# Optimization experiments

Hardware: AMD Instinct MI355X
Metric: run time of the kernel (lower is better)

## Reference

```python
import jax, jax.numpy as jnp
import numpy as np

DIM = 768
NUM_HEADS = 12
HEAD_DIM = DIM // NUM_HEADS
SCALE = HEAD_DIM ** -0.5


def setup_inputs() -> dict:
    key = jax.random.key(0)
    ks = jax.random.split(key, 12)
    B, N, C, H = 8, 1024, DIM, NUM_HEADS
    s = 0.02
    return {
        'q_in': jax.random.normal(ks[0], (B, N, C), jnp.float32),
        'kv_in': jax.random.normal(ks[1], (B, N, C), jnp.float32),
        'Wq': jax.random.normal(ks[2], (C, C), jnp.float32) * s,
        'Wk': jax.random.normal(ks[3], (C, C), jnp.float32) * s,
        'Wv': jax.random.normal(ks[4], (C, C), jnp.float32) * s,
        'Wp': jax.random.normal(ks[5], (C, C), jnp.float32) * s,
        'bp': jnp.zeros((C,), jnp.float32),
        'W_dy2': jax.random.normal(ks[6], (H, C), jnp.float32) * s,  # lf gate linear (out=H)
        'b_dy2': jnp.zeros((H,), jnp.float32),
        'W_dy': jax.random.normal(ks[7], (H, C), jnp.float32) * s,   # hf gate linear
        'b_dy': jnp.zeros((H,), jnp.float32),
        'lf_gamma': jnp.full((C,), 1e-5, jnp.float32),
        'hf_gamma': jnp.full((C,), 1e-5, jnp.float32),
        'star_scale': jnp.ones((1,), jnp.float32),
        'star_bias': jnp.zeros((1,), jnp.float32),
    }


def reference(q_in, kv_in, Wq, Wk, Wv, Wp, bp, W_dy2, b_dy2, W_dy, b_dy,
              lf_gamma, hf_gamma, star_scale, star_bias):
    B, Nq, C = q_in.shape
    Nk = kv_in.shape[1]
    H, D = NUM_HEADS, HEAD_DIM

    # StarReLU on query tokens (ignore_cls_token = 0)
    dy_feat = star_scale * jnp.square(jax.nn.relu(q_in)) + star_bias  # (B,Nq,C)

    # low-freq dynamic gate: tanh(linear) per head, repeated over head_dim
    dy_lf = jnp.tanh(jnp.einsum('bnc,hc->bnh', dy_feat, W_dy2) + b_dy2)  # (B,Nq,H)
    dy_lf = jnp.repeat(dy_lf, D, axis=-1)  # (B,Nq,C)

    # high-freq dynamic gate: rational-of-softplus^2
    dy = jax.nn.softplus(jnp.einsum('bnc,hc->bnh', dy_feat, W_dy) + b_dy)
    dy2 = jnp.square(dy)
    dy_hf = 2.0 * dy2 / (dy2 + 0.3678)
    dy_hf = jnp.repeat(dy_hf, D, axis=-1)  # (B,Nq,C)

    # projections (torch Linear: y = x @ W.T), split heads
    q = jnp.einsum('bnc,dc->bnd', q_in, Wq).reshape(B, Nq, H, D).transpose(0, 2, 1, 3)
    k = jnp.einsum('bnc,dc->bnd', kv_in, Wk).reshape(B, Nk, H, D).transpose(0, 2, 1, 3)
    v = jnp.einsum('bnc,dc->bnd', kv_in, Wv).reshape(B, Nk, H, D).transpose(0, 2, 1, 3)

    attn = jnp.einsum('bhqd,bhkd->bhqk', q * SCALE, k)
    attn = jax.nn.softmax(attn, axis=-1)
    x_attn = jnp.einsum('bhqk,bhkd->bhqd', attn, v)
    x_attn = x_attn.transpose(0, 2, 1, 3).reshape(B, Nq, C)

    # Nk == Nq branch: per-token residual high-frequency component
    v_reshape = v.transpose(0, 2, 1, 3).reshape(B, Nk, C)
    v_hf = v_reshape - x_attn

    x_attn = x_attn + x_attn * dy_lf * lf_gamma
    x_attn = x_attn + dy_hf * v_hf * hf_gamma

    out = jnp.einsum('bnc,dc->bnd', x_attn, Wp) + bp
    return out
```

## Files before the change

kernel.cpp:

```cpp
#include <hip/hip_runtime.h>
#include <hip/hip_bf16.h>
#include <stdint.h>

typedef unsigned short u16;
typedef unsigned int u32;
typedef unsigned long long u64;
typedef __attribute__((ext_vector_type(8))) short short8;
typedef __attribute__((ext_vector_type(4))) float f32x4;

#define LOG2E 1.44269504f

static __device__ __forceinline__ u16 f2bf(float f) {
    u32 x = __float_as_uint(f);
    u32 r = (x + 0x7FFFu + ((x >> 16) & 1u)) >> 16;
    return (u16)r;
}
static __device__ __forceinline__ float bf2f(u16 u) {
    return __uint_as_float(((u32)u) << 16);
}
static __device__ __forceinline__ u32 pk2(float lo, float hi) {
    __hip_bfloat162 t = __float22bfloat162_rn(float2{lo, hi});
    union { __hip_bfloat162 b; u32 u; } cv;
    cv.b = t;
    return cv.u;
}
static __device__ __forceinline__ float fexp2(float x) {
#if __has_builtin(__builtin_amdgcn_exp2f)
    return __builtin_amdgcn_exp2f(x);
#else
    return exp2f(x);
#endif
}

static __device__ __forceinline__ void g2l16(const void* g, void* l) {
    __builtin_amdgcn_global_load_lds((const __attribute__((address_space(1))) void*)g,
                                     (__attribute__((address_space(3))) void*)l, 16, 0, 0);
}

__global__ __launch_bounds__(256) void k_cvt_all(
    const float* __restrict__ q_in, const float* __restrict__ kv_in,
    const float* __restrict__ Wq, const float* __restrict__ Wk,
    const float* __restrict__ Wv, const float* __restrict__ Wp,
    const float* __restrict__ Wdy2, const float* __restrict__ Wdy,
    u16* __restrict__ qbf, u16* __restrict__ kvbf, u16* __restrict__ Wqb,
    u16* __restrict__ Wkb, u16* __restrict__ Wvb, u16* __restrict__ Wpb,
    u16* __restrict__ wgb) {
    int i = blockIdx.x * 256 + threadIdx.x;
    const float* src;
    u16* dst;
    int so, dofs;
    if (i < 786432) { src = q_in; dst = qbf; so = i; dofs = i; }
    else if (i < 1572864) { src = kv_in; dst = kvbf; so = i - 786432; dofs = so; }
    else if (i < 1646592) { src = Wq; dst = Wqb; so = i - 1572864; dofs = so; }
    else if (i < 1720320) { src = Wk; dst = Wkb; so = i - 1646592; dofs = so; }
    else if (i < 1794048) { src = Wv; dst = Wvb; so = i - 1720320; dofs = so; }
    else if (i < 1867776) { src = Wp; dst = Wpb; so = i - 1794048; dofs = so; }
    else if (i < 1870080) {
        int e = i - 1867776;
        dst = wgb; dofs = e;
        if (e < 1152) { src = Wdy2; so = e; }
        else { src = Wdy; so = e - 1152; }
    } else return;
    const float4* p = (const float4*)src + (size_t)so * 2;
    float4 a = p[0], b = p[1];
    short8 o;
    o[0] = f2bf(a.x); o[1] = f2bf(a.y); o[2] = f2bf(a.z); o[3] = f2bf(a.w);
    o[4] = f2bf(b.x); o[5] = f2bf(b.y); o[6] = f2bf(b.z); o[7] = f2bf(b.w);
    *((short8*)dst + dofs) = o;
}

__global__ __launch_bounds__(64) void k_gates(
    const u16* __restrict__ qbf, const u16* __restrict__ wgb,
    const float* __restrict__ bdy2, const float* __restrict__ bdy,
    const float* __restrict__ star_s, const float* __restrict__ star_b,
    float* __restrict__ glf, float* __restrict__ ghf) {
    int lane = threadIdx.x;
    int g = lane >> 4, c = lane & 15;
    int row0 = blockIdx.x * 16;
    float ss = star_s[0], sb = star_b[0];
    f32x4 acc[2];
    acc[0] = (f32x4){0.f, 0.f, 0.f, 0.f};
    acc[1] = (f32x4){0.f, 0.f, 0.f, 0.f};
    for (int t = 0; t < 24; ++t) {
        int k0 = t * 32;
        short8 x8 = *(const short8*)(qbf + (size_t)(row0 + c) * 768 + k0 + g * 8);
        float f[8];
#pragma unroll
        for (int j = 0; j < 8; ++j) {
            float x = fmaxf(bf2f((u16)x8[j]), 0.f);
            f[j] = ss * x * x + sb;
        }
        union { u32 u[4]; short8 s8; } au;
#pragma unroll
        for (int j = 0; j < 4; ++j) au.u[j] = pk2(f[2 * j], f[2 * j + 1]);
        short8 b0 = *(const short8*)(wgb + (size_t)c * 768 + k0 + g * 8);
        short8 b1 = (short8){0, 0, 0, 0, 0, 0, 0, 0};
        if (c < 8)
            b1 = *(const short8*)(wgb + (size_t)(16 + c) * 768 + k0 + g * 8);
        acc[0] = __builtin_amdgcn_mfma_f32_16x16x32_bf16(au.s8, b0, acc[0], 0, 0, 0);
        acc[1] = __builtin_amdgcn_mfma_f32_16x16x32_bf16(au.s8, b1, acc[1], 0, 0, 0);
    }
#pragma unroll
    for (int n = 0; n < 2; ++n)
#pragma unroll
        for (int r = 0; r < 4; ++r) {
            int token = row0 + g * 4 + r;
            int o = n * 16 + c;
            float v = acc[n][r];
            if (o < 12) {
                glf[(size_t)token * 12 + o] = tanhf(v + bdy2[o]);
            } else if (o < 24) {
                float x = v + bdy[o - 12];
                float sp = (x > 15.f) ? x : log1pf(expf(x));
                float d2 = sp * sp;
                ghf[(size_t)token * 12 + (o - 12)] = 2.f * d2 / (d2 + 0.3678f);
            }
        }
}

__device__ __forceinline__ void gemm_core(const u16* __restrict__ A,
                                          const u16* __restrict__ W, u16* As,
                                          u16* Bs, int rowA0, int rowB0,
                                          int lane, int w, int wm, int wn,
                                          f32x4 acc[4][4]) {
    int g = lane >> 4, c = lane & 15;
#pragma unroll
    for (int m = 0; m < 4; ++m)
#pragma unroll
        for (int n = 0; n < 4; ++n) acc[m][n] = (f32x4){0.f, 0.f, 0.f, 0.f};

    auto stage = [&](int buf, int k0) {
#pragma unroll
        for (int j = 0; j < 2; ++j) {
            int L = w * 128 + j * 64 + lane;
            int p = L >> 3, s8 = L & 7;
            int t2 = s8 ^ (p & 7);
            int row = 2 * p + (t2 >> 2);
            int chunk = t2 & 3;
            size_t go = (size_t)row * 768 + k0 + chunk * 8;
            g2l16(A + (size_t)rowA0 * 768 + go, As + buf * 4096 + L * 8);
            g2l16(W + (size_t)rowB0 * 768 + go, Bs + buf * 4096 + L * 8);
        }
    };

    stage(0, 0);
    stage(1, 32);
    int cur = 0, nxt = 2;
    for (int t = 0; t < 24; ++t) {
        if (t < 23) asm volatile("s_waitcnt vmcnt(4)" ::: "memory");
        else        asm volatile("s_waitcnt vmcnt(0)" ::: "memory");
        __builtin_amdgcn_s_barrier();
        if (t < 22) stage(nxt, (t + 2) * 32);
        short8 a[4], b[4];
#pragma unroll
        for (int m = 0; m < 4; ++m) {
            int row = wm * 64 + m * 16 + c;
            int off = (row >> 1) * 64 +
                      ((((row & 1) << 2) | g) ^ ((row >> 1) & 7)) * 8;
            a[m] = *(const short8*)(As + cur * 4096 + off);
        }
#pragma unroll
        for (int n = 0; n < 4; ++n) {
            int row = wn * 64 + n * 16 + c;
            int off = (row >> 1) * 64 +
                      ((((row & 1) << 2) | g) ^ ((row >> 1) & 7)) * 8;
            b[n] = *(const short8*)(Bs + cur * 4096 + off);
        }
        __builtin_amdgcn_s_setprio(1);
#pragma unroll
        for (int m = 0; m < 4; ++m)
#pragma unroll
            for (int n = 0; n < 4; ++n)
                acc[m][n] = __builtin_amdgcn_mfma_f32_16x16x32_bf16(
                    a[m], b[n], acc[m][n], 0, 0, 0);
        __builtin_amdgcn_s_setprio(0);
        cur = (cur == 2) ? 0 : cur + 1;
        nxt = (nxt == 2) ? 0 : nxt + 1;
    }
}

__global__ __launch_bounds__(256, 3) void k_gemm_qkv(
    const u16* __restrict__ qbf, const u16* __restrict__ kvbf,
    const u16* __restrict__ Wqb, const u16* __restrict__ Wkb,
    const u16* __restrict__ Wvb, u16* __restrict__ Qb, u16* __restrict__ Kb,
    u16* __restrict__ VTg, u16* __restrict__ vlin) {
    __shared__ __align__(16) u16 smem[24576];
    u16* As = smem;
    u16* Bs = smem + 12288;
    int bid = blockIdx.x;
    int logical = (bid & 7) * 144 + (bid >> 3);
    int panel = logical / 18, sub = logical % 18;
    int type = sub / 6, tn = sub % 6;
    int tid = threadIdx.x, lane = tid & 63, w = tid >> 6;
    int g = lane >> 4, c = lane & 15;
    int wm = w >> 1, wn = w & 1;
    int rowA0 = panel * 128, rowB0 = tn * 128;
    const u16* A = (type == 0) ? qbf : kvbf;
    const u16* W = (type == 0) ? Wqb : (type == 1) ? Wkb : Wvb;

    f32x4 acc[4][4];
    gemm_core(A, W, As, Bs, rowA0, rowB0, lane, w, wm, wn, acc);

    if (type == 0) {
        const float scl = 0.125f * LOG2E;
#pragma unroll
        for (int m = 0; m < 4; ++m)
#pragma unroll
            for (int n = 0; n < 4; ++n)
#pragma unroll
                for (int r = 0; r < 4; ++r) {
                    int row = rowA0 + wm * 64 + m * 16 + g * 4 + r;
                    int col = rowB0 + wn * 64 + n * 16 + c;
                    int bb = row >> 10, nn = row & 1023, hh = col >> 6,
                        dd = col & 63;
                    Qb[((size_t)(bb * 12 + hh) << 16) + (nn << 6) + dd] =
                        f2bf(acc[m][n][r] * scl);
                }
    } else if (type == 1) {
#pragma unroll
        for (int m = 0; m < 4; ++m)
#pragma unroll
            for (int n = 0; n < 4; ++n)
#pragma unroll
                for (int r = 0; r < 4; ++r) {
                    int row = rowA0 + wm * 64 + m * 16 + g * 4 + r;
                    int col = rowB0 + wn * 64 + n * 16 + c;
                    int bb = row >> 10, nn = row & 1023, hh = col >> 6,
                        dd = col & 63;
                    Kb[((size_t)(bb * 12 + hh) << 16) + (nn << 6) + dd] =
                        f2bf(acc[m][n][r]);
                }
    } else {
#pragma unroll
        for (int m = 0; m < 4; ++m)
#pragma unroll
            for (int n = 0; n < 4; ++n)
#pragma unroll
                for (int r = 0; r < 4; ++r) {
                    int row = rowA0 + wm * 64 + m * 16 + g * 4 + r;
                    int col = rowB0 + wn * 64 + n * 16 + c;
                    vlin[(size_t)row * 768 + col] = f2bf(acc[m][n][r]);
                }
        __syncthreads();
#pragma unroll
        for (int m = 0; m < 4; ++m)
#pragma unroll
            for (int n = 0; n < 4; ++n)
#pragma unroll
                for (int r = 0; r < 4; ++r) {
                    int rl = wm * 64 + m * 16 + g * 4 + r;
                    int cl = wn * 64 + n * 16 + c;
                    smem[cl * 128 + rl] = f2bf(acc[m][n][r]);
                }
        __syncthreads();
        int bb = rowA0 >> 10, nn0 = rowA0 & 1023;
#pragma unroll
        for (int j = 0; j < 8; ++j) {
            int idx = j * 256 + tid;
            int rT = idx >> 4, cc = idx & 15;
            int dout = rowB0 + rT, hh = dout >> 6, dd = dout & 63;
            const u16* srow = smem + rT * 128 + cc * 8;
            size_t robase = ((size_t)(bb * 12 + hh) * 64 + dd) * 1024;
#pragma unroll
            for (int e2 = 0; e2 < 4; ++e2) {
                int n0 = nn0 + cc * 8 + 2 * e2;
                int t6 = n0 & 63;
                int pos = (((t6 >> 1) & 1) << 5) | (((t6 >> 2) & 3) << 3) |
                          (((t6 >> 4) & 3) << 1) | (t6 & 1);
                u32 val = (u32)srow[2 * e2] | ((u32)srow[2 * e2 + 1] << 16);
                *(u32*)(VTg + robase + (n0 & ~63) + pos) = val;
            }
        }
    }
}

__global__ __launch_bounds__(256, 3) void k_gemm_out(
    const u16* __restrict__ xf, const u16* __restrict__ Wpb,
    const float* __restrict__ bp, float* __restrict__ out) {
    __shared__ __align__(16) u16 smem[24576];
    u16* As = smem;
    u16* Bs = smem + 12288;
    int bid = blockIdx.x;
    int logical = (bid & 7) * 48 + (bid >> 3);
    int c48 = logical % 48;
    int tm = (logical / 48) * 8 + c48 / 6, tn = c48 % 6;
    int tid = threadIdx.x, lane = tid & 63, w = tid >> 6;
    int wm = w >> 1, wn = w & 1;
    int rowA0 = tm * 128, rowB0 = tn * 128;

    f32x4 acc[4][4];
    gemm_core(xf, Wpb, As, Bs, rowA0, rowB0, lane, w, wm, wn, acc);

#pragma unroll
    for (int m = 0; m < 4; ++m)
#pragma unroll
        for (int n = 0; n < 4; ++n)
#pragma unroll
            for (int r = 0; r < 4; ++r) {
                int row = rowA0 + wm * 64 + m * 16 + (lane >> 4) * 4 + r;
                int col = rowB0 + wn * 64 + n * 16 + (lane & 15);
                out[(size_t)row * 768 + col] = acc[m][n][r] + bp[col];
            }
}

__global__ __launch_bounds__(256, 3) void k_attn(
    const u16* __restrict__ Qb, const u16* __restrict__ Kb,
    const u16* __restrict__ VTg, const u16* __restrict__ vlin,
    const float* __restrict__ glf, const float* __restrict__ ghf,
    const float* __restrict__ lfg, const float* __restrict__ hfg,
    u16* __restrict__ xfinal) {
    __shared__ __align__(16) u16 Ks[12288];
    __shared__ __align__(16) u16 Vs[12288];
    int b8 = blockIdx.x;
    int sw = (b8 & 7) * 96 + (b8 >> 3);
    int bh = sw >> 3, qblk = sw & 7;
    int bb = bh / 12, hh = bh % 12;
    int tid = threadIdx.x, lane = tid & 63, w = tid >> 6;
    int g = lane >> 4, c = lane & 15;
    const char* Kp = (const char*)(Kb + ((size_t)bh << 16));
    const char* Vp = (const char*)(VTg + ((size_t)bh << 16));
    const u16* Qp = Qb + ((size_t)bh << 16);
    int q0 = qblk * 128 + w * 32;

    short8 qf[2][2];
#pragma unroll
    for (int qb = 0; qb < 2; ++qb)
#pragma unroll
        for (int ks = 0; ks < 2; ++ks)
            qf[qb][ks] = *(const short8*)(Qp + (size_t)(q0 + qb * 16 + c) * 64 +
                                          ks * 32 + g * 8);

    f32x4 o[2][4];
#pragma unroll
    for (int qb = 0; qb < 2; ++qb)
#pragma unroll
        for (int n = 0; n < 4; ++n) o[qb][n] = (f32x4){0.f, 0.f, 0.f, 0.f};
    f32x4 o5[2];
    o5[0] = (f32x4){0.f, 0.f, 0.f, 0.f};
    o5[1] = (f32x4){0.f, 0.f, 0.f, 0.f};
    const short8 vones = (short8){(short)0x3F80, (short)0x3F80, (short)0x3F80,
                                  (short)0x3F80, (short)0x3F80, (short)0x3F80,
                                  (short)0x3F80, (short)0x3F80};

    int kgo[2], vgo[2], ldo[2];
#pragma unroll
    for (int h = 0; h < 2; ++h) {
        int idx = w * 64 + lane + h * 256;
        int row = idx >> 3;
        int colb = ((idx & 7) * 16) ^ ((row & 7) << 4);
        kgo[h] = row * 128 + colb;
        vgo[h] = row * 2048 + colb;
        ldo[h] = (w * 64 + h * 256) * 16;
    }

    auto stage = [&](int bi, int t) {
#pragma unroll
        for (int h = 0; h < 2; ++h) {
            g2l16(Kp + (size_t)t * 8192 + kgo[h], (char*)Ks + bi * 8192 + ldo[h]);
            g2l16(Vp + (size_t)t * 128 + vgo[h], (char*)Vs + bi * 8192 + ldo[h]);
        }
    };

    stage(0, 0);
    stage(1, 1);
    int cur = 0, nxt = 2;
    int cs = (c & 7) << 4;
    for (int t = 0; t < 16; ++t) {
        if (t < 15) asm volatile("s_waitcnt vmcnt(4)" ::: "memory");
        else        asm volatile("s_waitcnt vmcnt(0)" ::: "memory");
        __builtin_amdgcn_s_barrier();
        if (t < 14) stage(nxt, t + 2);
        const char* Kbase = (const char*)Ks + cur * 8192;
        const char* Vbase = (const char*)Vs + cur * 8192;
        short8 kf[4][2], vf[4][2];
#pragma unroll
        for (int m = 0; m < 4; ++m) {
            int rowb = (m * 16 + c) * 128;
#pragma unroll
            for (int ks = 0; ks < 2; ++ks)
                kf[m][ks] = *(const short8*)(Kbase + rowb +
                                             ((g * 16 + ks * 64) ^ cs));
        }
#pragma unroll
        for (int n = 0; n < 4; ++n) {
            int rowb = (n * 16 + c) * 128;
#pragma unroll
            for (int a = 0; a < 2; ++a)
                vf[n][a] = *(const short8*)(Vbase + rowb +
                                            ((a * 64 + g * 16) ^ cs));
        }
#pragma unroll
        for (int qb = 0; qb < 2; ++qb) {
            f32x4 s[4];
            __builtin_amdgcn_s_setprio(1);
#pragma unroll
            for (int m = 0; m < 4; ++m) {
                s[m] = __builtin_amdgcn_mfma_f32_16x16x32_bf16(
                    kf[m][0], qf[qb][0], (f32x4){0.f, 0.f, 0.f, 0.f}, 0, 0, 0);
                s[m] = __builtin_amdgcn_mfma_f32_16x16x32_bf16(
                    kf[m][1], qf[qb][1], s[m], 0, 0, 0);
            }
            __builtin_amdgcn_s_setprio(0);
            u32 P2[4][2];
#pragma unroll
            for (int m = 0; m < 4; ++m) {
#pragma unroll
                for (int r = 0; r < 4; ++r) s[m][r] = fexp2(s[m][r]);
                P2[m][0] = pk2(s[m][0], s[m][1]);
                P2[m][1] = pk2(s[m][2], s[m][3]);
            }
#pragma unroll
            for (int a = 0; a < 2; ++a) {
                union { u32 u[4]; short8 s8; } pu;
                pu.u[0] = P2[0][a]; pu.u[1] = P2[1][a];
                pu.u[2] = P2[2][a]; pu.u[3] = P2[3][a];
                __builtin_amdgcn_s_setprio(1);
#pragma unroll
                for (int n = 0; n < 4; ++n)
                    o[qb][n] = __builtin_amdgcn_mfma_f32_16x16x32_bf16(
                        pu.s8, vf[n][a], o[qb][n], 0, 0, 0);
                o5[qb] = __builtin_amdgcn_mfma_f32_16x16x32_bf16(
                    pu.s8, vones, o5[qb], 0, 0, 0);
                __builtin_amdgcn_s_setprio(0);
            }
        }
        cur = (cur == 2) ? 0 : cur + 1;
        nxt = (nxt == 2) ? 0 : nxt + 1;
    }
    __syncthreads();

    u16* X = &Ks[0];
#pragma unroll
    for (int qb = 0; qb < 2; ++qb) {
        float rl[4];
#pragma unroll
        for (int r = 0; r < 4; ++r) rl[r] = 1.0f / o5[qb][r];
#pragma unroll
        for (int n = 0; n < 4; ++n)
#pragma unroll
            for (int r = 0; r < 4; ++r) {
                int row = w * 32 + qb * 16 + 4 * g + r;
                int col = n * 16 + c;
                int byte = row * 128 + ((col * 2) ^ ((row & 3) << 4));
                *(u16*)((char*)X + byte) = f2bf(o[qb][n][r] * rl[r]);
            }
    }
    __syncthreads();
    {
        int row = tid >> 1, half = tid & 1;
        size_t token = (size_t)bb * 1024 + qblk * 128 + row;
        float alf = glf[token * 12 + hh];
        float ahf = ghf[token * 12 + hh];
        int dbase = hh * 64 + half * 32;
        const u16* vbase = vlin + token * 768 + dbase;
        u16* obase = xfinal + token * 768 + dbase;
#pragma unroll
        for (int j = 0; j < 4; ++j) {
            int phys = ((half * 4 + j) ^ (row & 3)) * 16;
            short8 xa8 = *(const short8*)((char*)X + row * 128 + phys);
            short8 vl8 = *(const short8*)(vbase + j * 8);
            float4 lg0 = *(const float4*)(lfg + dbase + j * 8);
            float4 lg1 = *(const float4*)(lfg + dbase + j * 8 + 4);
            float4 hg0 = *(const float4*)(hfg + dbase + j * 8);
            float4 hg1 = *(const float4*)(hfg + dbase + j * 8 + 4);
            float lg[8] = {lg0.x, lg0.y, lg0.z, lg0.w, lg1.x, lg1.y, lg1.z, lg1.w};
            float hg[8] = {hg0.x, hg0.y, hg0.z, hg0.w, hg1.x, hg1.y, hg1.z, hg1.w};
            short8 oo;
#pragma unroll
            for (int e = 0; e < 8; ++e) {
                float xa = bf2f((u16)xa8[e]);
                float v = bf2f((u16)vl8[e]);
                float val = xa + xa * alf * lg[e] + ahf * (v - xa) * hg[e];
                oo[e] = f2bf(val);
            }
            *(short8*)(obase + j * 8) = oo;
        }
    }
}

extern "C" void kernel_launch(void* const* d_in, const int* in_sizes, int n_in,
                              void* d_out, int out_size, void* d_ws,
                              size_t ws_size, hipStream_t stream) {
    const float* q_in = (const float*)d_in[0];
    const float* kv_in = (const float*)d_in[1];
    const float* Wq = (const float*)d_in[2];
    const float* Wk = (const float*)d_in[3];
    const float* Wv = (const float*)d_in[4];
    const float* Wp = (const float*)d_in[5];
    const float* bp = (const float*)d_in[6];
    const float* Wdy2 = (const float*)d_in[7];
    const float* bdy2 = (const float*)d_in[8];
    const float* Wdy = (const float*)d_in[9];
    const float* bdy = (const float*)d_in[10];
    const float* lfg = (const float*)d_in[11];
    const float* hfg = (const float*)d_in[12];
    const float* st_s = (const float*)d_in[13];
    const float* st_b = (const float*)d_in[14];
    float* out = (float*)d_out;

    char* ws = (char*)d_ws;
    const size_t MC2 = (size_t)8192 * 768 * 2;
    const size_t WB = (size_t)768 * 768 * 2;
    u16* qbf = (u16*)(ws);
    u16* kvbf = (u16*)(ws + MC2);
    u16* Wqb = (u16*)(ws + 2 * MC2);
    u16* Wkb = (u16*)(ws + 2 * MC2 + WB);
    u16* Wvb = (u16*)(ws + 2 * MC2 + 2 * WB);
    u16* Wpb = (u16*)(ws + 2 * MC2 + 3 * WB);
    u16* Qb = (u16*)(ws + 2 * MC2 + 4 * WB);
    u16* Kb = (u16*)(ws + 3 * MC2 + 4 * WB);
    u16* VTg = (u16*)(ws + 4 * MC2 + 4 * WB);
    u16* vlin = (u16*)(ws + 5 * MC2 + 4 * WB);
    float* glf = (float*)(ws + 6 * MC2 + 4 * WB);
    float* ghf = (float*)(ws + 6 * MC2 + 4 * WB + (size_t)8192 * 12 * 4);
    u16* wgb = (u16*)(ws + 6 * MC2 + 4 * WB + (size_t)8192 * 12 * 8);
    u16* xfinal = qbf;

    k_cvt_all<<<7305, 256, 0, stream>>>(q_in, kv_in, Wq, Wk, Wv, Wp, Wdy2,
                                        Wdy, qbf, kvbf, Wqb, Wkb, Wvb, Wpb,
                                        wgb);
    k_gates<<<512, 64, 0, stream>>>(qbf, wgb, bdy2, bdy, st_s, st_b, glf, ghf);
    k_gemm_qkv<<<1152, 256, 0, stream>>>(qbf, kvbf, Wqb, Wkb, Wvb, Qb, Kb,
                                         VTg, vlin);
    k_attn<<<768, 256, 0, stream>>>(Qb, Kb, VTg, vlin, glf, ghf, lfg, hfg,
                                    xfinal);
    k_gemm_out<<<384, 256, 0, stream>>>(xfinal, Wpb, bp, out);
}
```

Before: 134.2 us.

## Fuse K and V projections to share kv_in tile loads in QKV GEMM

The K and V projection blocks now run together: each block loads one kv_in A tile and multiplies it against both Wk and Wv tiles, keeping two accumulator sets, so the kv_in activations are read once instead of twice. The grid shrinks from 1152 to 768 blocks. The GEMM pipeline also changes from triple-buffered prefetch with one barrier to double buffering with two barriers per k-step, and launch bounds drop from 3 to 2 blocks per SM. The doubled accumulators raise register pressure and lower occupancy, and the extra barrier may cost latency hiding in both the QKV and output GEMMs.

```diff
diff --git a/kernel.cpp b/kernel.cpp
--- a/kernel.cpp
+++ b/kernel.cpp
@@ -118,16 +118,17 @@
         }
 }
 
-__device__ __forceinline__ void gemm_core(const u16* __restrict__ A,
-                                          const u16* __restrict__ W, u16* As,
-                                          u16* Bs, int rowA0, int rowB0,
-                                          int lane, int w, int wm, int wn,
-                                          f32x4 acc[4][4]) {
+template <int NB>
+__device__ __forceinline__ void gemm_nb(const u16* __restrict__ A,
+                                        const u16* __restrict__ W0,
+                                        const u16* __restrict__ W1, u16* smem,
+                                        int rowA0, int rowB0, int lane, int w,
+                                        int wm, int wn, f32x4 acc0[4][4],
+                                        f32x4 acc1[4][4]) {
     int g = lane >> 4, c = lane & 15;
-#pragma unroll
-    for (int m = 0; m < 4; ++m)
-#pragma unroll
-        for (int n = 0; n < 4; ++n) acc[m][n] = (f32x4){0.f, 0.f, 0.f, 0.f};
+    u16* As = smem;
+    u16* B0 = smem + 8192;
+    u16* B1 = smem + 16384;
 
     auto stage = [&](int buf, int k0) {
 #pragma unroll
@@ -139,69 +140,88 @@
             int chunk = t2 & 3;
             size_t go = (size_t)row * 768 + k0 + chunk * 8;
             g2l16(A + (size_t)rowA0 * 768 + go, As + buf * 4096 + L * 8);
-            g2l16(W + (size_t)rowB0 * 768 + go, Bs + buf * 4096 + L * 8);
+            g2l16(W0 + (size_t)rowB0 * 768 + go, B0 + buf * 4096 + L * 8);
+            if (NB == 2)
+                g2l16(W1 + (size_t)rowB0 * 768 + go, B1 + buf * 4096 + L * 8);
         }
     };
 
     stage(0, 0);
-    stage(1, 32);
-    int cur = 0, nxt = 2;
+    int buf = 0;
     for (int t = 0; t < 24; ++t) {
-        if (t < 23) asm volatile("s_waitcnt vmcnt(4)" ::: "memory");
-        else        asm volatile("s_waitcnt vmcnt(0)" ::: "memory");
+        if (t < 23) stage(buf ^ 1, (t + 1) * 32);
+        if (t < 23) {
+            if (NB == 2) asm volatile("s_waitcnt vmcnt(6)" ::: "memory");
+            else         asm volatile("s_waitcnt vmcnt(4)" ::: "memory");
+        } else {
+            asm volatile("s_waitcnt vmcnt(0)" ::: "memory");
+        }
         __builtin_amdgcn_s_barrier();
-        if (t < 22) stage(nxt, (t + 2) * 32);
-        short8 a[4], b[4];
+        short8 a[4], b0[4], b1[4];
 #pragma unroll
         for (int m = 0; m < 4; ++m) {
             int row = wm * 64 + m * 16 + c;
             int off = (row >> 1) * 64 +
                       ((((row & 1) << 2) | g) ^ ((row >> 1) & 7)) * 8;
-            a[m] = *(const short8*)(As + cur * 4096 + off);
+            a[m] = *(const short8*)(As + buf * 4096 + off);
         }
 #pragma unroll
         for (int n = 0; n < 4; ++n) {
             int row = wn * 64 + n * 16 + c;
             int off = (row >> 1) * 64 +
                       ((((row & 1) << 2) | g) ^ ((row >> 1) & 7)) * 8;
-            b[n] = *(const short8*)(Bs + cur * 4096 + off);
+            b0[n] = *(const short8*)(B0 + buf * 4096 + off);
+            if (NB == 2) b1[n] = *(const short8*)(B1 + buf * 4096 + off);
         }
         __builtin_amdgcn_s_setprio(1);
 #pragma unroll
         for (int m = 0; m < 4; ++m)
 #pragma unroll
             for (int n = 0; n < 4; ++n)
-                acc[m][n] = __builtin_amdgcn_mfma_f32_16x16x32_bf16(
-                    a[m], b[n], acc[m][n], 0, 0, 0);
+                acc0[m][n] = __builtin_amdgcn_mfma_f32_16x16x32_bf16(
+                    a[m], b0[n], acc0[m][n], 0, 0, 0);
+        if (NB == 2) {
+#pragma unroll
+            for (int m = 0; m < 4; ++m)
+#pragma unroll
+                for (int n = 0; n < 4; ++n)
+                    acc1[m][n] = __builtin_amdgcn_mfma_f32_16x16x32_bf16(
+                        a[m], b1[n], acc1[m][n], 0, 0, 0);
+        }
         __builtin_amdgcn_s_setprio(0);
-        cur = (cur == 2) ? 0 : cur + 1;
-        nxt = (nxt == 2) ? 0 : nxt + 1;
-    }
-}
-
-__global__ __launch_bounds__(256, 3) void k_gemm_qkv(
+        __builtin_amdgcn_s_barrier();
+        buf ^= 1;
+    }
+}
+
+__global__ __launch_bounds__(256, 2) void k_gemm_qkv(
     const u16* __restrict__ qbf, const u16* __restrict__ kvbf,
     const u16* __restrict__ Wqb, const u16* __restrict__ Wkb,
     const u16* __restrict__ Wvb, u16* __restrict__ Qb, u16* __restrict__ Kb,
     u16* __restrict__ VTg, u16* __restrict__ vlin) {
     __shared__ __align__(16) u16 smem[24576];
-    u16* As = smem;
-    u16* Bs = smem + 12288;
     int bid = blockIdx.x;
-    int logical = (bid & 7) * 144 + (bid >> 3);
-    int panel = logical / 18, sub = logical % 18;
-    int type = sub / 6, tn = sub % 6;
+    int logical = (bid & 7) * 96 + (bid >> 3);
+    int panel = logical / 12, sub = logical % 12;
+    bool isQ = (sub < 6);
+    int tn = sub % 6;
     int tid = threadIdx.x, lane = tid & 63, w = tid >> 6;
     int g = lane >> 4, c = lane & 15;
     int wm = w >> 1, wn = w & 1;
     int rowA0 = panel * 128, rowB0 = tn * 128;
-    const u16* A = (type == 0) ? qbf : kvbf;
-    const u16* W = (type == 0) ? Wqb : (type == 1) ? Wkb : Wvb;
-
-    f32x4 acc[4][4];
-    gemm_core(A, W, As, Bs, rowA0, rowB0, lane, w, wm, wn, acc);
-
-    if (type == 0) {
+
+    f32x4 acc0[4][4], acc1[4][4];
+#pragma unroll
+    for (int m = 0; m < 4; ++m)
+#pragma unroll
+        for (int n = 0; n < 4; ++n) {
+            acc0[m][n] = (f32x4){0.f, 0.f, 0.f, 0.f};
+            acc1[m][n] = (f32x4){0.f, 0.f, 0.f, 0.f};
+        }
+
+    if (isQ) {
+        gemm_nb<1>(qbf, Wqb, Wqb, smem, rowA0, rowB0, lane, w, wm, wn, acc0,
+                   acc1);
         const float scl = 0.125f * LOG2E;
 #pragma unroll
         for (int m = 0; m < 4; ++m)
@@ -214,9 +234,11 @@
                     int bb = row >> 10, nn = row & 1023, hh = col >> 6,
                         dd = col & 63;
                     Qb[((size_t)(bb * 12 + hh) << 16) + (nn << 6) + dd] =
-                        f2bf(acc[m][n][r] * scl);
+                        f2bf(acc0[m][n][r] * scl);
                 }
-    } else if (type == 1) {
+    } else {
+        gemm_nb<2>(kvbf, Wkb, Wvb, smem, rowA0, rowB0, lane, w, wm, wn, acc0,
+                   acc1);
 #pragma unroll
         for (int m = 0; m < 4; ++m)
 #pragma unroll
@@ -228,18 +250,8 @@
                     int bb = row >> 10, nn = row & 1023, hh = col >> 6,
                         dd = col & 63;
                     Kb[((size_t)(bb * 12 + hh) << 16) + (nn << 6) + dd] =
-                        f2bf(acc[m][n][r]);
-                }
-    } else {
-#pragma unroll
-        for (int m = 0; m < 4; ++m)
-#pragma unroll
-            for (int n = 0; n < 4; ++n)
-#pragma unroll
-                for (int r = 0; r < 4; ++r) {
-                    int row = rowA0 + wm * 64 + m * 16 + g * 4 + r;
-                    int col = rowB0 + wn * 64 + n * 16 + c;
-                    vlin[(size_t)row * 768 + col] = f2bf(acc[m][n][r]);
+                        f2bf(acc0[m][n][r]);
+                    vlin[(size_t)row * 768 + col] = f2bf(acc1[m][n][r]);
                 }
         __syncthreads();
 #pragma unroll
@@ -250,7 +262,7 @@
                 for (int r = 0; r < 4; ++r) {
                     int rl = wm * 64 + m * 16 + g * 4 + r;
                     int cl = wn * 64 + n * 16 + c;
-                    smem[cl * 128 + rl] = f2bf(acc[m][n][r]);
+                    smem[cl * 128 + rl] = f2bf(acc1[m][n][r]);
                 }
         __syncthreads();
         int bb = rowA0 >> 10, nn0 = rowA0 & 1023;
@@ -274,32 +286,38 @@
     }
 }
 
-__global__ __launch_bounds__(256, 3) void k_gemm_out(
+__global__ __launch_bounds__(256, 2) void k_gemm_out(
     const u16* __restrict__ xf, const u16* __restrict__ Wpb,
     const float* __restrict__ bp, float* __restrict__ out) {
     __shared__ __align__(16) u16 smem[24576];
-    u16* As = smem;
-    u16* Bs = smem + 12288;
     int bid = blockIdx.x;
     int logical = (bid & 7) * 48 + (bid >> 3);
     int c48 = logical % 48;
     int tm = (logical / 48) * 8 + c48 / 6, tn = c48 % 6;
     int tid = threadIdx.x, lane = tid & 63, w = tid >> 6;
+    int g = lane >> 4, c = lane & 15;
     int wm = w >> 1, wn = w & 1;
     int rowA0 = tm * 128, rowB0 = tn * 128;
 
-    f32x4 acc[4][4];
-    gemm_core(xf, Wpb, As, Bs, rowA0, rowB0, lane, w, wm, wn, acc);
-
+    f32x4 acc0[4][4], acc1[4][4];
 #pragma unroll
     for (int m = 0; m < 4; ++m)
 #pragma unroll
+        for (int n = 0; n < 4; ++n) {
+            acc0[m][n] = (f32x4){0.f, 0.f, 0.f, 0.f};
+            acc1[m][n] = (f32x4){0.f, 0.f, 0.f, 0.f};
+        }
+    gemm_nb<1>(xf, Wpb, Wpb, smem, rowA0, rowB0, lane, w, wm, wn, acc0, acc1);
+
+#pragma unroll
+    for (int m = 0; m < 4; ++m)
+#pragma unroll
         for (int n = 0; n < 4; ++n)
 #pragma unroll
             for (int r = 0; r < 4; ++r) {
-                int row = rowA0 + wm * 64 + m * 16 + (lane >> 4) * 4 + r;
-                int col = rowB0 + wn * 64 + n * 16 + (lane & 15);
-                out[(size_t)row * 768 + col] = acc[m][n][r] + bp[col];
+                int row = rowA0 + wm * 64 + m * 16 + g * 4 + r;
+                int col = rowB0 + wn * 64 + n * 16 + c;
+                out[(size_t)row * 768 + col] = acc0[m][n][r] + bp[col];
             }
 }
 
@@ -520,8 +538,8 @@
                                         Wdy, qbf, kvbf, Wqb, Wkb, Wvb, Wpb,
                                         wgb);
     k_gates<<<512, 64, 0, stream>>>(qbf, wgb, bdy2, bdy, st_s, st_b, glf, ghf);
-    k_gemm_qkv<<<1152, 256, 0, stream>>>(qbf, kvbf, Wqb, Wkb, Wvb, Qb, Kb,
-                                         VTg, vlin);
+    k_gemm_qkv<<<768, 256, 0, stream>>>(qbf, kvbf, Wqb, Wkb, Wvb, Qb, Kb,
+                                        VTg, vlin);
     k_attn<<<768, 256, 0, stream>>>(Qb, Kb, VTg, vlin, glf, ghf, lfg, hfg,
                                     xfinal);
     k_gemm_out<<<384, 256, 0, stream>>>(xfinal, Wpb, bp, out);
```

Measured after the change: 138.6 us. 1.03x slower.
